# Kernel optimization log

Hardware: AMD Instinct MI355X
Metric: run time of the kernel (lower is better)

The kernel has to match this reference:

```python
import jax, jax.numpy as jnp
import numpy as np

N = 4096
K = 64
E = N * K
LD = 2      # location_dim
ED = 8      # attention embed_dim
H = 256     # lck_structure width
BN_EPS = 1e-5


def setup_inputs() -> dict:
    key = jax.random.key(0)
    ks = jax.random.split(key, 12)
    coor = jax.random.normal(ks[0], (E, 2 * LD), dtype=jnp.float32)
    row = jnp.repeat(jnp.arange(N, dtype=jnp.int64), K)
    col = jax.random.randint(ks[1], (E,), 0, N, dtype=jnp.int64)
    sparse_idx = jnp.stack([row, col], axis=0)
    geodesic = jax.random.uniform(ks[2], (N, N), dtype=jnp.float32)
    angle_ratio = jax.random.uniform(ks[3], (N, N), dtype=jnp.float32)
    # LocalConditionalKer params: Linear(4,H), Linear(H,H), BN(H), Linear(H,1)
    W0 = jax.random.normal(ks[4], (2 * LD, H), dtype=jnp.float32) / np.sqrt(2 * LD)
    b0 = jnp.zeros((H,), jnp.float32)
    W1 = jax.random.normal(ks[5], (H, H), dtype=jnp.float32) / np.sqrt(H)
    b1 = jnp.zeros((H,), jnp.float32)
    gamma = jnp.ones((H,), jnp.float32)
    beta = jnp.zeros((H,), jnp.float32)
    W2 = jax.random.normal(ks[6], (H, 1), dtype=jnp.float32) / np.sqrt(H)
    b2 = jnp.zeros((1,), jnp.float32)
    # Attention params: query/key Linear(LD, ED)
    Wq = jax.random.normal(ks[7], (LD, ED), dtype=jnp.float32) / np.sqrt(LD)
    bq = jnp.zeros((ED,), jnp.float32)
    Wk = jax.random.normal(ks[8], (LD, ED), dtype=jnp.float32) / np.sqrt(LD)
    bk = jnp.zeros((ED,), jnp.float32)
    x = jax.random.normal(ks[9], (1,), dtype=jnp.float32)
    return dict(x=x, coor=coor, sparse_idx=sparse_idx, geodesic=geodesic,
                angle_ratio=angle_ratio, W0=W0, b0=b0, W1=W1, b1=b1,
                gamma=gamma, beta=beta, W2=W2, b2=b2,
                Wq=Wq, bq=bq, Wk=Wk, bk=bk)


def _lck(coor, W0, b0, W1, b1, gamma, beta, W2, b2):
    # loop semantics: activation applied before every layer except j==1
    h = jnp.tanh(coor) @ W0 + b0          # j=0: Linear(4,H)
    h = h @ W1 + b1                        # j=1: Linear(H,H), no pre-activation
    h = jnp.tanh(h)                        # j=2: BN(H) in training mode (batch stats)
    mu = jnp.mean(h, axis=0)
    var = jnp.var(h, axis=0)               # biased variance, as torch BN uses
    h = gamma * (h - mu) * jax.lax.rsqrt(var + BN_EPS) + beta
    h = jnp.tanh(h) @ W2 + b2              # j=3: Linear(H,1)
    return jax.nn.relu(h)                  # [E,1]


def reference(x, coor, sparse_idx, geodesic, angle_ratio,
              W0, b0, W1, b1, gamma, beta, W2, b2, Wq, bq, Wk, bk):
    row, col = sparse_idx[0], sparse_idx[1]
    # per-edge kernel value, scattered into dense NxN (duplicates summed)
    vals = _lck(coor, W0, b0, W1, b1, gamma, beta, W2, b2).reshape(-1)  # [E]
    lcker = jnp.zeros((N, N), vals.dtype).at[row, col].add(vals)
    # attention over neighbors
    sphere = coor[:, :LD] + coor[:, LD:]           # [E, 2]
    sphere = sphere.reshape(N, K, LD)               # [N, K, 2]
    center = sphere[:, :1, :]                       # [N, 1, 2]
    q = center @ Wq + bq                            # [N, 1, ED]
    k = sphere @ Wk + bk                            # [N, K, ED]
    att = jnp.abs(jnp.einsum('nqe,nke->nqk', q, k).squeeze(1))  # [N, K]
    alpha = jnp.zeros((N, N), att.dtype).at[row, col].add(att.reshape(-1))
    distance_decay = jnp.exp(-alpha * geodesic)
    return lcker * distance_decay * angle_ratio
```

## Files before the change

### kernel.cpp

```cpp
#include <hip/hip_runtime.h>

#define N_ 4096
#define K_ 64
#define E_ (N_*K_)
#define H_ 256
#define EPS_ 1e-5f
#define L2E_ 1.4426950408889634f
#define TL2E_ 2.8853900817779268f

#if __has_builtin(__builtin_amdgcn_exp2f)
#define EXP2(x) __builtin_amdgcn_exp2f(x)
#else
#define EXP2(x) __expf((x) * 0.6931471805599453f)
#endif

__device__ __forceinline__ float ftanh(float x) {
    float e = EXP2(x * TL2E_);
    return 1.0f - 2.0f * __builtin_amdgcn_rcpf(e + 1.0f);
}

__global__ __launch_bounds__(256) void prep_kernel(
    const float* __restrict__ W0, const float* __restrict__ b0,
    const float* __restrict__ W1, const float* __restrict__ b1,
    float* __restrict__ W01, float* __restrict__ b01)
{
    int c = threadIdx.x;
    int h0 = blockIdx.x * 8;
    float a0 = 0.f, a1 = 0.f, a2 = 0.f, a3 = 0.f, ab = 0.f;
    #pragma unroll
    for (int h = h0; h < h0 + 8; ++h) {
        float w = W1[h * H_ + c];
        a0 = fmaf(W0[0 * H_ + h], w, a0);
        a1 = fmaf(W0[1 * H_ + h], w, a1);
        a2 = fmaf(W0[2 * H_ + h], w, a2);
        a3 = fmaf(W0[3 * H_ + h], w, a3);
        ab = fmaf(b0[h], w, ab);
    }
    if (blockIdx.x == 0) ab += b1[c];
    atomicAdd(&W01[c], a0);
    atomicAdd(&W01[H_ + c], a1);
    atomicAdd(&W01[2 * H_ + c], a2);
    atomicAdd(&W01[3 * H_ + c], a3);
    atomicAdd(&b01[c], ab);
}

__global__ __launch_bounds__(256, 8) void stats_kernel(
    const float* __restrict__ coor, const float* __restrict__ W01,
    const float* __restrict__ b01, float* __restrict__ part)
{
    const int c = threadIdx.x;
    const float w0 = TL2E_ * W01[c],        w1 = TL2E_ * W01[H_ + c];
    const float w2 = TL2E_ * W01[2*H_ + c], w3 = TL2E_ * W01[3*H_ + c];
    const float bb = TL2E_ * b01[c];
    __shared__ float4 T[128];
    const int e0 = blockIdx.x * 128;
    if (c < 128) {
        float4 v = reinterpret_cast<const float4*>(coor)[e0 + c];
        T[c] = make_float4(ftanh(v.x), ftanh(v.y), ftanh(v.z), ftanh(v.w));
    }
    __syncthreads();
    float sr = 0.f, sr2 = 0.f;
    #pragma unroll 8
    for (int i = 0; i < 128; ++i) {
        float4 t = T[i];
        float u = fmaf(t.w, w3, fmaf(t.z, w2, fmaf(t.y, w1, fmaf(t.x, w0, bb))));
        float r = __builtin_amdgcn_rcpf(EXP2(u) + 1.0f);
        sr += r;
        sr2 = fmaf(r, r, sr2);
    }
    part[blockIdx.x * 512 + c] = sr;
    part[blockIdx.x * 512 + 256 + c] = sr2;
}

__global__ __launch_bounds__(512) void reduce_kernel(
    const float* __restrict__ part, float* __restrict__ sums)
{
    int t = threadIdx.x;
    int b0 = blockIdx.x * 64;
    float local = 0.f;
    #pragma unroll 8
    for (int b = b0; b < b0 + 64; ++b) local += part[b * 512 + t];
    atomicAdd(&sums[t], local);
}

__global__ __launch_bounds__(256) void finalize_kernel(
    const float* __restrict__ sums, const float* __restrict__ gamma,
    const float* __restrict__ beta, const float* __restrict__ W2,
    const float* __restrict__ b2,
    const float* __restrict__ W01, const float* __restrict__ b01,
    float* __restrict__ folded, float* __restrict__ swp)
{
    int c = threadIdx.x;
    const float inv = 1.0f / (float)E_;
    float p = sums[c] * inv;
    float q = sums[256 + c] * inv;
    float mu = 1.0f - 2.0f * p;
    float var = 4.0f * fmaf(-p, p, q);
    float a = gamma[c] * rsqrtf(var + EPS_);
    float bf = fmaf(-mu, a, beta[c]);
    folded[c * 8 + 0] = TL2E_ * W01[c];
    folded[c * 8 + 1] = TL2E_ * W01[H_ + c];
    folded[c * 8 + 2] = TL2E_ * W01[2 * H_ + c];
    folded[c * 8 + 3] = TL2E_ * W01[3 * H_ + c];
    folded[c * 8 + 4] = TL2E_ * b01[c];
    folded[c * 8 + 5] = -4.0f * L2E_ * a;
    folded[c * 8 + 6] = TL2E_ * (a + bf);
    folded[c * 8 + 7] = -2.0f * W2[c];
    __shared__ float red[256];
    red[c] = W2[c];
    __syncthreads();
    for (int s = 128; s > 0; s >>= 1) {
        if (c < s) red[c] += red[c + s];
        __syncthreads();
    }
    if (c == 0) swp[0] = red[0] + b2[0];
}

__global__ __launch_bounds__(256, 8) void edge_kernel(
    const float* __restrict__ coor, const int* __restrict__ idx,
    const float* __restrict__ folded, const float* __restrict__ swp,
    const float* __restrict__ Wq, const float* __restrict__ bq,
    const float* __restrict__ Wk, const float* __restrict__ bk,
    const float* __restrict__ geo, const float* __restrict__ ang,
    float* __restrict__ out)
{
    __shared__ float4 FS[2 * H_];
    __shared__ float accbuf[4][64];
    const int t = threadIdx.x;
    {
        const float4* F = reinterpret_cast<const float4*>(folded);
        FS[t] = F[t];
        FS[t + 256] = F[t + 256];
    }
    const int w = t >> 6, lane = t & 63;
    const int rloc = w >> 1, half = w & 1;
    const int row = blockIdx.x * 2 + rloc;
    const int e = row * K_ + lane;

    {
        float4 z = make_float4(0.f, 0.f, 0.f, 0.f);
        float4* orow = reinterpret_cast<float4*>(out + (size_t)row * N_);
        #pragma unroll
        for (int i = 0; i < 8; ++i) orow[half * 512 + i * 64 + lane] = z;
    }

    const int col = idx[E_ + e];
    float4 ce = reinterpret_cast<const float4*>(coor)[e];
    float ex = ce.x + ce.z, ey = ce.y + ce.w;
    float sx = __shfl(ex, 0), sy = __shfl(ey, 0);
    float att = 0.f;
    #pragma unroll
    for (int j = 0; j < 8; ++j) {
        float qj = fmaf(sy, Wq[8 + j], fmaf(sx, Wq[j], bq[j]));
        float kj = fmaf(ey, Wk[8 + j], fmaf(ex, Wk[j], bk[j]));
        att = fmaf(qj, kj, att);
    }
    att = fabsf(att);

    float t0 = ftanh(ce.x), t1 = ftanh(ce.y), t2 = ftanh(ce.z), t3 = ftanh(ce.w);

    __syncthreads();

    const float4* Fp = &FS[half * 256];
    float acc = 0.f;
    #pragma unroll 4
    for (int i = 0; i < 128; ++i) {
        float4 f0 = Fp[2 * i];
        float4 f1 = Fp[2 * i + 1];
        float u = fmaf(t3, f0.w, fmaf(t2, f0.z, fmaf(t1, f0.y, fmaf(t0, f0.x, f1.x))));
        float r  = __builtin_amdgcn_rcpf(EXP2(u) + 1.0f);
        float r2 = __builtin_amdgcn_rcpf(EXP2(fmaf(r, f1.y, f1.z)) + 1.0f);
        acc = fmaf(r2, f1.w, acc);
    }
    accbuf[w][lane] = acc;
    __syncthreads();

    if (half == 0) {
        float val = fmaxf(accbuf[2 * rloc][lane] + accbuf[2 * rloc + 1][lane] + swp[0], 0.f);
        float vsum = val, asum = att;
        bool leader = true;
        for (int j = 0; j < 64; ++j) {
            int   bc = __shfl(col, j);
            float bv = __shfl(val, j);
            float ba = __shfl(att, j);
            if (bc == col && j != lane) {
                if (j < lane) leader = false;
                else { vsum += bv; asum += ba; }
            }
        }
        if (leader) {
            size_t p = (size_t)row * N_ + col;
            out[p] = vsum * __expf(-asum * geo[p]) * ang[p];
        }
    }
}

extern "C" void kernel_launch(void* const* d_in, const int* in_sizes, int n_in,
                              void* d_out, int out_size, void* d_ws, size_t ws_size,
                              hipStream_t stream)
{
    const float* coor  = (const float*)d_in[1];
    const int*   idx   = (const int*)d_in[2];
    const float* geo   = (const float*)d_in[3];
    const float* ang   = (const float*)d_in[4];
    const float* W0    = (const float*)d_in[5];
    const float* b0    = (const float*)d_in[6];
    const float* W1    = (const float*)d_in[7];
    const float* b1    = (const float*)d_in[8];
    const float* gamma = (const float*)d_in[9];
    const float* beta  = (const float*)d_in[10];
    const float* W2    = (const float*)d_in[11];
    const float* b2    = (const float*)d_in[12];
    const float* Wq    = (const float*)d_in[13];
    const float* bq    = (const float*)d_in[14];
    const float* Wk    = (const float*)d_in[15];
    const float* bk    = (const float*)d_in[16];

    float* ws = (float*)d_ws;
    float* sums   = ws;
    float* W01    = ws + 512;
    float* b01    = ws + 1536;
    float* folded = ws + 1792;
    float* swp    = ws + 3840;
    float* part   = ws + 4096;

    hipMemsetAsync(ws, 0, 1792 * sizeof(float), stream);

    prep_kernel<<<32, 256, 0, stream>>>(W0, b0, W1, b1, W01, b01);
    stats_kernel<<<E_ / 128, 256, 0, stream>>>(coor, W01, b01, part);
    reduce_kernel<<<32, 512, 0, stream>>>(part, sums);
    finalize_kernel<<<1, 256, 0, stream>>>(sums, gamma, beta, W2, b2, W01, b01,
                                           folded, swp);
    edge_kernel<<<N_ / 2, 256, 0, stream>>>(coor, idx, folded, swp,
                                            Wq, bq, Wk, bk, geo, ang, (float*)d_out);
}
```

Before: 79.72 us.

## Register-block four edges per thread to reuse folded weights in edge kernel

The edge kernel's hidden-unit loop now gives each thread four edges across a 32-unit chunk, where before each thread handled one edge across 128 units. Each LDS read of folded weights is therefore reused for four edges, and the four independent exp/rcp chains add instruction-level parallelism. Tanh of the inputs and the sphere sums are computed once per edge into shared memory, and partials from eight chunks are reduced through a shared array. This uses more shared memory and registers, and the attention and dedup tail now runs on only two waves.

```diff
diff --git a/kernel.cpp b/kernel.cpp
--- a/kernel.cpp
+++ b/kernel.cpp
@@ -125,58 +125,72 @@
     float* __restrict__ out)
 {
     __shared__ float4 FS[2 * H_];
-    __shared__ float accbuf[4][64];
+    __shared__ float4 TS[128];
+    __shared__ float2 EXY[128];
+    __shared__ float  ACC[8][128];
+
     const int t = threadIdx.x;
+    const int row0 = blockIdx.x * 2;
     {
         const float4* F = reinterpret_cast<const float4*>(folded);
         FS[t] = F[t];
         FS[t + 256] = F[t + 256];
     }
-    const int w = t >> 6, lane = t & 63;
-    const int rloc = w >> 1, half = w & 1;
-    const int row = blockIdx.x * 2 + rloc;
-    const int e = row * K_ + lane;
-
+    if (t < 128) {
+        float4 ce = reinterpret_cast<const float4*>(coor)[row0 * K_ + t];
+        TS[t] = make_float4(ftanh(ce.x), ftanh(ce.y), ftanh(ce.z), ftanh(ce.w));
+        EXY[t] = make_float2(ce.x + ce.z, ce.y + ce.w);
+    }
     {
         float4 z = make_float4(0.f, 0.f, 0.f, 0.f);
-        float4* orow = reinterpret_cast<float4*>(out + (size_t)row * N_);
+        float4* orow = reinterpret_cast<float4*>(out + (size_t)row0 * N_);
         #pragma unroll
-        for (int i = 0; i < 8; ++i) orow[half * 512 + i * 64 + lane] = z;
-    }
-
-    const int col = idx[E_ + e];
-    float4 ce = reinterpret_cast<const float4*>(coor)[e];
-    float ex = ce.x + ce.z, ey = ce.y + ce.w;
-    float sx = __shfl(ex, 0), sy = __shfl(ey, 0);
-    float att = 0.f;
-    #pragma unroll
-    for (int j = 0; j < 8; ++j) {
-        float qj = fmaf(sy, Wq[8 + j], fmaf(sx, Wq[j], bq[j]));
-        float kj = fmaf(ey, Wk[8 + j], fmaf(ex, Wk[j], bk[j]));
-        att = fmaf(qj, kj, att);
-    }
-    att = fabsf(att);
-
-    float t0 = ftanh(ce.x), t1 = ftanh(ce.y), t2 = ftanh(ce.z), t3 = ftanh(ce.w);
-
-    __syncthreads();
-
-    const float4* Fp = &FS[half * 256];
-    float acc = 0.f;
+        for (int i = 0; i < 8; ++i) orow[i * 256 + t] = z;
+    }
+    __syncthreads();
+
+    const int eg = (t & 31) * 4;
+    const int chunk = t >> 5;
+    const float4 tq0 = TS[eg], tq1 = TS[eg + 1], tq2 = TS[eg + 2], tq3 = TS[eg + 3];
+    const float4* Fp = &FS[chunk * 64];
+    float a0 = 0.f, a1 = 0.f, a2 = 0.f, a3 = 0.f;
     #pragma unroll 4
-    for (int i = 0; i < 128; ++i) {
+    for (int i = 0; i < 32; ++i) {
         float4 f0 = Fp[2 * i];
         float4 f1 = Fp[2 * i + 1];
-        float u = fmaf(t3, f0.w, fmaf(t2, f0.z, fmaf(t1, f0.y, fmaf(t0, f0.x, f1.x))));
-        float r  = __builtin_amdgcn_rcpf(EXP2(u) + 1.0f);
-        float r2 = __builtin_amdgcn_rcpf(EXP2(fmaf(r, f1.y, f1.z)) + 1.0f);
-        acc = fmaf(r2, f1.w, acc);
-    }
-    accbuf[w][lane] = acc;
-    __syncthreads();
-
-    if (half == 0) {
-        float val = fmaxf(accbuf[2 * rloc][lane] + accbuf[2 * rloc + 1][lane] + swp[0], 0.f);
+        #define EVAL(tq, ak) { \
+            float u = fmaf(tq.w, f0.w, fmaf(tq.z, f0.z, fmaf(tq.y, f0.y, fmaf(tq.x, f0.x, f1.x)))); \
+            float r = __builtin_amdgcn_rcpf(EXP2(u) + 1.0f); \
+            float r2 = __builtin_amdgcn_rcpf(EXP2(fmaf(r, f1.y, f1.z)) + 1.0f); \
+            ak = fmaf(r2, f1.w, ak); }
+        EVAL(tq0, a0) EVAL(tq1, a1) EVAL(tq2, a2) EVAL(tq3, a3)
+        #undef EVAL
+    }
+    *reinterpret_cast<float4*>(&ACC[chunk][eg]) = make_float4(a0, a1, a2, a3);
+    __syncthreads();
+
+    const int w = t >> 6, lane = t & 63;
+    if (w < 2) {
+        const int row = row0 + w;
+        const int eb = w * 64 + lane;
+        float val = swp[0];
+        #pragma unroll
+        for (int c = 0; c < 8; ++c) val += ACC[c][eb];
+        val = fmaxf(val, 0.f);
+
+        float2 exy = EXY[eb];
+        float ex = exy.x, ey = exy.y;
+        float sx = __shfl(ex, 0), sy = __shfl(ey, 0);
+        float att = 0.f;
+        #pragma unroll
+        for (int j = 0; j < 8; ++j) {
+            float qj = fmaf(sy, Wq[8 + j], fmaf(sx, Wq[j], bq[j]));
+            float kj = fmaf(ey, Wk[8 + j], fmaf(ex, Wk[j], bk[j]));
+            att = fmaf(qj, kj, att);
+        }
+        att = fabsf(att);
+
+        const int col = idx[E_ + row * K_ + lane];
         float vsum = val, asum = att;
         bool leader = true;
         for (int j = 0; j < 64; ++j) {
```

Result: faster. 77.70 us (-2.5%).
